# Kernel tuning notes

Hardware: AMD Instinct MI355X
Metric: run time of the kernel (lower is better)

Reference implementation:

```python
import jax, jax.numpy as jnp
import numpy as np

N = 16384        # num_nodes (64 graphs x 256 nodes, consecutive blocks)
G = 64           # num_graphs = len(nodes_per_graph)
GENES = 12132    # num_genes (hardcoded in source)
E = 262144       # edges, avg degree 16
PER = 256        # nodes per graph


def setup_inputs() -> dict:
    key = jax.random.key(0)
    ks = jax.random.split(key, 12)
    x = jax.random.normal(ks[0], (N, GENES), dtype=jnp.float32)
    edge_index = jax.random.randint(ks[1], (2, E), 0, N, dtype=jnp.int32)
    # node i belongs to graph i // PER  (consecutive-block partition as in the source loop)
    graph_ids = jnp.repeat(jnp.arange(G, dtype=jnp.int32), PER)
    node_scales = jax.random.uniform(ks[2], (GENES,), dtype=jnp.float32, minval=0.5, maxval=1.5)
    gcn_weight = jax.random.normal(ks[3], (GENES, G), dtype=jnp.float32) / np.float32(np.sqrt(GENES))
    gcn_bias = jax.random.normal(ks[4], (G,), dtype=jnp.float32) * 0.01
    w1 = jax.random.normal(ks[5], (G, N), dtype=jnp.float32) / np.float32(np.sqrt(N))   # to_graph_layer [out,in]
    b1 = jax.random.normal(ks[6], (G,), dtype=jnp.float32) * 0.01
    final_means = jax.random.normal(ks[7], (G,), dtype=jnp.float32)
    final_scales = jax.random.uniform(ks[8], (G,), dtype=jnp.float32, minval=0.5, maxval=1.5)
    w2 = jax.random.normal(ks[9], (1, G), dtype=jnp.float32) / np.float32(np.sqrt(G))   # to_final_layer
    b2 = jax.random.normal(ks[10], (1,), dtype=jnp.float32) * 0.01
    return {
        "x": x, "edge_index": edge_index, "graph_ids": graph_ids,
        "node_scales": node_scales, "gcn_weight": gcn_weight, "gcn_bias": gcn_bias,
        "w1": w1, "b1": b1, "final_means": final_means, "final_scales": final_scales,
        "w2": w2, "b2": b2,
    }


def reference(x, edge_index, graph_ids, node_scales, gcn_weight, gcn_bias,
              w1, b1, final_means, final_scales, w2, b2):
    n = x.shape[0]
    x = x / node_scales                              # [N, GENES]
    xw = x @ gcn_weight                              # [N, G]  GCNConv linear (normalize=False)
    src, dst = edge_index[0], edge_index[1]
    # message passing: sum x_j over in-edges; '+ xw' realizes the explicitly-added self loops
    agg = jax.ops.segment_sum(xw[src], dst, num_segments=n) + xw + gcn_bias  # [N, G]
    # per-graph gather: node i takes column graph_ids[i] (vectorized form of the source loop)
    selected = jnp.take_along_axis(agg, graph_ids[:, None], axis=1)[:, 0]    # [N]
    # NOTE: the (selected - graph_means)/graph_scales in the source is dead code
    # (immediately overwritten by `x = selected_outputs`), so it is omitted.
    h = w1 @ selected + b1                           # [G]
    h = (h - final_means) / final_scales
    out = w2 @ h + b2                                # [1]
    return jax.nn.sigmoid(out)
```

## Files before the change

### kernel.cpp

```cpp
#include <hip/hip_runtime.h>
#include <hip/hip_bf16.h>

typedef unsigned short u16;
typedef unsigned int   u32;
typedef __attribute__((ext_vector_type(8))) short bf16x8;
typedef __attribute__((ext_vector_type(4))) float f32x4;
typedef __attribute__((ext_vector_type(4))) u32   u32x4;

#define GENES  12132
#define KPAD   12160
#define NROW   16384
#define GCOL   64
#define KTAIL  12096
#define CHUNKS32 380
#define KSPLIT 5
#define CPW    76

__device__ __forceinline__ u32 pack_hi(float x, float y) {
  return __builtin_amdgcn_perm(__float_as_uint(y), __float_as_uint(x), 0x07060302u);
}
__device__ __forceinline__ u32 pack_lo(float x, float y) {
  float lx = x - __uint_as_float(__float_as_uint(x) & 0xFFFF0000u);
  float ly = y - __uint_as_float(__float_as_uint(y) & 0xFFFF0000u);
  return pack_hi(lx, ly);
}
__device__ __forceinline__ void cvt8(const float* __restrict__ p, bf16x8& h8, bf16x8& l8) {
  const f32x4 a = *(const f32x4*)p;
  const f32x4 b = *(const f32x4*)(p + 4);
  u32x4 hv = { pack_hi(a[0], a[1]), pack_hi(a[2], a[3]),
               pack_hi(b[0], b[1]), pack_hi(b[2], b[3]) };
  u32x4 lv = { pack_lo(a[0], a[1]), pack_lo(a[2], a[3]),
               pack_lo(b[0], b[1]), pack_lo(b[2], b[3]) };
  h8 = __builtin_bit_cast(bf16x8, hv);
  l8 = __builtin_bit_cast(bf16x8, lv);
}

__global__ __launch_bounds__(256) void prep_all(
    const float* __restrict__ gw, const float* __restrict__ ns,
    const float* __restrict__ x,
    u16* __restrict__ Wth, u16* __restrict__ Wtl,
    float* __restrict__ xpad, float* __restrict__ hbuf) {
  const int bid = blockIdx.x;
  const int t   = threadIdx.x;
  if (bid < KPAD / 64) {
    __shared__ u16 th[64 * 72];
    __shared__ u16 tl[64 * 72];
    const int k0 = bid * 64;
#pragma unroll
    for (int i = 0; i < 16; ++i) {
      int idx = i * 256 + t;
      int k = idx >> 6, c = idx & 63;
      int gk = k0 + k;
      float wv = 0.f;
      if (gk < GENES) wv = gw[(size_t)gk * GCOL + c] / ns[gk];
      u32 u = __float_as_uint(wv);
      float lf = wv - __uint_as_float(u & 0xFFFF0000u);
      th[c * 72 + k] = (u16)(u >> 16);
      tl[c * 72 + k] = (u16)(__float_as_uint(lf) >> 16);
    }
    __syncthreads();
    const int c  = t >> 2;
    const int kk = (t & 3) * 16;
    uint4 a0 = *(const uint4*)(th + c * 72 + kk);
    uint4 a1 = *(const uint4*)(th + c * 72 + kk + 8);
    uint4 b0 = *(const uint4*)(tl + c * 72 + kk);
    uint4 b1 = *(const uint4*)(tl + c * 72 + kk + 8);
    *(uint4*)(Wth + (size_t)c * KPAD + k0 + kk)     = a0;
    *(uint4*)(Wth + (size_t)c * KPAD + k0 + kk + 8) = a1;
    *(uint4*)(Wtl + (size_t)c * KPAD + k0 + kk)     = b0;
    *(uint4*)(Wtl + (size_t)c * KPAD + k0 + kk + 8) = b1;
  } else {
    int i = (bid - KPAD / 64) * 256 + t;
    int row = i >> 6, col = i & 63;
    float v = 0.f;
    if (col < GENES - KTAIL) v = x[(size_t)row * GENES + KTAIL + col];
    xpad[i] = v;
    if (bid == KPAD / 64 && t < 64) hbuf[t] = 0.f;
  }
}

__global__ __launch_bounds__(64) void gemm_kernel(
    const float* __restrict__ x, const float* __restrict__ xpad,
    const u16* __restrict__ Wth, const u16* __restrict__ Wtl,
    float* __restrict__ xwp) {
  const int wid = blockIdx.x;
  const int sp  = wid >> 8;
  const int rg  = wid & 255;
  const int l   = threadIdx.x;
  const int lr  = l & 15;
  const int kq  = l >> 4;

  const int r0 = rg * 64;

  f32x4 acc[4][4];
#pragma unroll
  for (int s = 0; s < 4; ++s)
#pragma unroll
    for (int c = 0; c < 4; ++c) acc[s][c] = (f32x4){0.f, 0.f, 0.f, 0.f};

  const u16* bh_base = Wth + (size_t)lr * KPAD + kq * 8;
  const u16* bl_base = Wtl + (size_t)lr * KPAD + kq * 8;
  const int gch0 = sp * CPW;

#pragma unroll 2
  for (int ci = 0; ci < CPW; ++ci) {
    const int gch = gch0 + ci;
    const int k0  = gch * 32;
    bf16x8 bh[4], bl[4];
#pragma unroll
    for (int cg = 0; cg < 4; ++cg) {
      bh[cg] = *(const bf16x8*)(bh_base + (size_t)cg * (16 * KPAD) + k0);
      bl[cg] = *(const bf16x8*)(bl_base + (size_t)cg * (16 * KPAD) + k0);
    }
    bf16x8 ah[4], al[4];
    if (gch < KTAIL / 32) {
#pragma unroll
      for (int s = 0; s < 4; ++s)
        cvt8(x + (size_t)(r0 + s * 16 + lr) * GENES + k0 + kq * 8, ah[s], al[s]);
    } else {
#pragma unroll
      for (int s = 0; s < 4; ++s)
        cvt8(xpad + (size_t)(r0 + s * 16 + lr) * 64 + (k0 - KTAIL) + kq * 8, ah[s], al[s]);
    }
#pragma unroll
    for (int s = 0; s < 4; ++s)
#pragma unroll
      for (int cg = 0; cg < 4; ++cg) {
        acc[s][cg] = __builtin_amdgcn_mfma_f32_16x16x32_bf16(ah[s], bh[cg], acc[s][cg], 0, 0, 0);
        acc[s][cg] = __builtin_amdgcn_mfma_f32_16x16x32_bf16(al[s], bh[cg], acc[s][cg], 0, 0, 0);
        acc[s][cg] = __builtin_amdgcn_mfma_f32_16x16x32_bf16(ah[s], bl[cg], acc[s][cg], 0, 0, 0);
      }
  }

  float* outp = xwp + (size_t)sp * NROW * GCOL;
#pragma unroll
  for (int s = 0; s < 4; ++s) {
    const int rbase = r0 + s * 16 + kq * 4;
#pragma unroll
    for (int cg = 0; cg < 4; ++cg) {
      const int col = cg * 16 + lr;
#pragma unroll
      for (int j = 0; j < 4; ++j)
        outp[(size_t)(rbase + j) * GCOL + col] = acc[s][cg][j];
    }
  }
}

__global__ __launch_bounds__(256) void reduce_sel(
    const f32x4* __restrict__ xwp, f32x4* __restrict__ xw4,
    const float* __restrict__ gb, float* __restrict__ sel) {
  int i = blockIdx.x * 256 + threadIdx.x;
  f32x4 v = xwp[i];
#pragma unroll
  for (int p = 1; p < KSPLIT; ++p) {
    f32x4 u = xwp[(size_t)p * (NROW * GCOL / 4) + i];
    v[0] += u[0]; v[1] += u[1]; v[2] += u[2]; v[3] += u[3];
  }
  xw4[i] = v;
  int row = i >> 4;
  int g = row >> 8;
  if ((i & 15) == (g >> 2)) sel[row] = v[g & 3] + gb[g];
}

__global__ __launch_bounds__(256) void edge_kernel(
    const int* __restrict__ ei, const float* __restrict__ xw,
    float* __restrict__ sel, int E) {
  int e = blockIdx.x * 256 + threadIdx.x;
  if (e < E) {
    int s = ei[e];
    int d = ei[E + e];
    int g = d >> 8;
    atomicAdd(&sel[d], xw[(size_t)s * GCOL + g]);
  }
}

__global__ __launch_bounds__(256) void hreduce_kernel(
    const float* __restrict__ w1, const float* __restrict__ sel,
    float* __restrict__ hbuf) {
  const int k = blockIdx.x >> 2;
  const int q = blockIdx.x & 3;
  const int t = threadIdx.x;
  const float4* wr = reinterpret_cast<const float4*>(w1 + (size_t)k * NROW);
  const float4* sv = reinterpret_cast<const float4*>(sel);
  float sum = 0.f;
#pragma unroll
  for (int i = 0; i < 4; ++i) {
    int idx = q * 1024 + i * 256 + t;
    float4 a = wr[idx];
    float4 b = sv[idx];
    sum += a.x * b.x + a.y * b.y + a.z * b.z + a.w * b.w;
  }
#pragma unroll
  for (int off = 32; off > 0; off >>= 1) sum += __shfl_down(sum, off, 64);
  __shared__ float wsum[4];
  if ((t & 63) == 0) wsum[t >> 6] = sum;
  __syncthreads();
  if (t == 0) atomicAdd(&hbuf[k], wsum[0] + wsum[1] + wsum[2] + wsum[3]);
}

__global__ void finalize_kernel(
    const float* __restrict__ hbuf, const float* __restrict__ b1,
    const float* __restrict__ fm, const float* __restrict__ fs,
    const float* __restrict__ w2, const float* __restrict__ b2,
    float* __restrict__ out) {
  int t = threadIdx.x;
  float h  = hbuf[t] + b1[t];
  float hn = (h - fm[t]) / fs[t];
  float v  = w2[t] * hn;
#pragma unroll
  for (int off = 32; off > 0; off >>= 1) v += __shfl_down(v, off, 64);
  if (t == 0) {
    float z = v + b2[0];
    out[0] = 1.f / (1.f + expf(-z));
  }
}

extern "C" void kernel_launch(void* const* d_in, const int* in_sizes, int n_in,
                              void* d_out, int out_size, void* d_ws, size_t ws_size,
                              hipStream_t stream) {
  const float* x    = (const float*)d_in[0];
  const int*   ei   = (const int*)d_in[1];
  const float* ns   = (const float*)d_in[3];
  const float* gw   = (const float*)d_in[4];
  const float* gb   = (const float*)d_in[5];
  const float* w1   = (const float*)d_in[6];
  const float* b1   = (const float*)d_in[7];
  const float* fm   = (const float*)d_in[8];
  const float* fs   = (const float*)d_in[9];
  const float* w2   = (const float*)d_in[10];
  const float* b2   = (const float*)d_in[11];
  float* out = (float*)d_out;

  const int E = in_sizes[1] / 2;

  float* ws   = (float*)d_ws;
  float* xw   = ws;
  float* sel  = xw + (size_t)NROW * GCOL;
  float* hbuf = sel + NROW;
  u16*   Wth  = (u16*)(hbuf + 64);
  u16*   Wtl  = Wth + (size_t)GCOL * KPAD;
  float* xpad = (float*)(Wtl + (size_t)GCOL * KPAD);
  float* xwp  = xpad + (size_t)NROW * 64;

  hipLaunchKernelGGL(prep_all, dim3(KPAD / 64 + NROW * 64 / 256), dim3(256), 0, stream,
                     gw, ns, x, Wth, Wtl, xpad, hbuf);
  hipLaunchKernelGGL(gemm_kernel, dim3(256 * KSPLIT), dim3(64), 0, stream,
                     x, xpad, Wth, Wtl, xwp);
  hipLaunchKernelGGL(reduce_sel, dim3(NROW * GCOL / 4 / 256), dim3(256), 0, stream,
                     (const f32x4*)xwp, (f32x4*)xw, gb, sel);
  hipLaunchKernelGGL(edge_kernel, dim3((E + 255) / 256), dim3(256), 0, stream,
                     ei, xw, sel, E);
  hipLaunchKernelGGL(hreduce_kernel, dim3(GCOL * 4), dim3(256), 0, stream,
                     w1, sel, hbuf);
  hipLaunchKernelGGL(finalize_kernel, dim3(1), dim3(64), 0, stream,
                     hbuf, b1, fm, fs, w2, b2, out);
}
```

Before: 345.7 us.

## Prefetch next A chunk into registers and double the K-split

The GEMM loop now loads the next 32-wide K chunk of x into registers before running the current chunk's MFMAs, so global-load latency overlaps with compute. The K dimension is also split into 10 slices instead of 5, giving twice as many workgroups for occupancy. In exchange there are more partial-sum buffers to reduce afterwards and higher register pressure from the prefetch registers. The first chunk's load always reads x directly, which is correct only if no split begins in the padded tail.

```diff
diff --git a/kernel.cpp b/kernel.cpp
--- a/kernel.cpp
+++ b/kernel.cpp
@@ -12,9 +12,8 @@
 #define NROW   16384
 #define GCOL   64
 #define KTAIL  12096
-#define CHUNKS32 380
-#define KSPLIT 5
-#define CPW    76
+#define KSPLIT 10
+#define CPW    38
 
 __device__ __forceinline__ u32 pack_hi(float x, float y) {
   return __builtin_amdgcn_perm(__float_as_uint(y), __float_as_uint(x), 0x07060302u);
@@ -24,9 +23,7 @@
   float ly = y - __uint_as_float(__float_as_uint(y) & 0xFFFF0000u);
   return pack_hi(lx, ly);
 }
-__device__ __forceinline__ void cvt8(const float* __restrict__ p, bf16x8& h8, bf16x8& l8) {
-  const f32x4 a = *(const f32x4*)p;
-  const f32x4 b = *(const f32x4*)(p + 4);
+__device__ __forceinline__ void cvt8v(f32x4 a, f32x4 b, bf16x8& h8, bf16x8& l8) {
   u32x4 hv = { pack_hi(a[0], a[1]), pack_hi(a[2], a[3]),
                pack_hi(b[0], b[1]), pack_hi(b[2], b[3]) };
   u32x4 lv = { pack_lo(a[0], a[1]), pack_lo(a[2], a[3]),
@@ -89,8 +86,7 @@
   const int l   = threadIdx.x;
   const int lr  = l & 15;
   const int kq  = l >> 4;
-
-  const int r0 = rg * 64;
+  const int r0  = rg * 64;
 
   f32x4 acc[4][4];
 #pragma unroll
@@ -98,13 +94,24 @@
 #pragma unroll
     for (int c = 0; c < 4; ++c) acc[s][c] = (f32x4){0.f, 0.f, 0.f, 0.f};
 
-  const u16* bh_base = Wth + (size_t)lr * KPAD + kq * 8;
-  const u16* bl_base = Wtl + (size_t)lr * KPAD + kq * 8;
-  const int gch0 = sp * CPW;
-
-#pragma unroll 2
+  const u16*   bh_base = Wth + (size_t)lr * KPAD + kq * 8;
+  const u16*   bl_base = Wtl + (size_t)lr * KPAD + kq * 8;
+  const float* xbase   = x    + (size_t)(r0 + lr) * GENES + kq * 8;
+  const float* pbase   = xpad + (size_t)(r0 + lr) * 64    + kq * 8;
+  const int    c0      = sp * CPW;
+
+  f32x4 an[8];
+  {
+    const float* p = xbase + c0 * 32;
+#pragma unroll
+    for (int s = 0; s < 4; ++s) {
+      an[2 * s]     = *(const f32x4*)(p + (size_t)s * 16 * GENES);
+      an[2 * s + 1] = *(const f32x4*)(p + (size_t)s * 16 * GENES + 4);
+    }
+  }
+
   for (int ci = 0; ci < CPW; ++ci) {
-    const int gch = gch0 + ci;
+    const int gch = c0 + ci;
     const int k0  = gch * 32;
     bf16x8 bh[4], bl[4];
 #pragma unroll
@@ -113,14 +120,25 @@
       bl[cg] = *(const bf16x8*)(bl_base + (size_t)cg * (16 * KPAD) + k0);
     }
     bf16x8 ah[4], al[4];
-    if (gch < KTAIL / 32) {
-#pragma unroll
-      for (int s = 0; s < 4; ++s)
-        cvt8(x + (size_t)(r0 + s * 16 + lr) * GENES + k0 + kq * 8, ah[s], al[s]);
-    } else {
-#pragma unroll
-      for (int s = 0; s < 4; ++s)
-        cvt8(xpad + (size_t)(r0 + s * 16 + lr) * 64 + (k0 - KTAIL) + kq * 8, ah[s], al[s]);
+#pragma unroll
+    for (int s = 0; s < 4; ++s) cvt8v(an[2 * s], an[2 * s + 1], ah[s], al[s]);
+    if (ci + 1 < CPW) {
+      const int ngch = gch + 1;
+      if (ngch < KTAIL / 32) {
+        const float* p = xbase + ngch * 32;
+#pragma unroll
+        for (int s = 0; s < 4; ++s) {
+          an[2 * s]     = *(const f32x4*)(p + (size_t)s * 16 * GENES);
+          an[2 * s + 1] = *(const f32x4*)(p + (size_t)s * 16 * GENES + 4);
+        }
+      } else {
+        const float* p = pbase + (ngch * 32 - KTAIL);
+#pragma unroll
+        for (int s = 0; s < 4; ++s) {
+          an[2 * s]     = *(const f32x4*)(p + (size_t)s * 16 * 64);
+          an[2 * s + 1] = *(const f32x4*)(p + (size_t)s * 16 * 64 + 4);
+        }
+      }
     }
 #pragma unroll
     for (int s = 0; s < 4; ++s)
```

Result: no change. 346.5 us (+0.2%).

## Pre-swizzle weight fragments, use 4-wave blocks with A prefetch and deeper K-split

Applied to the files above, without the earlier changes.

The bf16 hi/lo weight split is now stored in MFMA-fragment order, so each lane does one contiguous 16-byte load per fragment instead of strided row reads. The GEMM moves from 64-thread blocks covering 64 rows to 256-thread blocks in which each wave covers 32 rows. The next A chunk is loaded before the current chunk's MFMAs are issued, and the K-split doubles to 10, which gives more blocks and more loads in flight for the memory-bound read of x. In exchange the partial-sum buffer and the reduce_sel traffic double, and the weight fragments are reloaded for every 32-row strip rather than every 64-row one.

```diff
diff --git a/kernel.cpp b/kernel.cpp
--- a/kernel.cpp
+++ b/kernel.cpp
@@ -12,9 +12,8 @@
 #define NROW   16384
 #define GCOL   64
 #define KTAIL  12096
-#define CHUNKS32 380
-#define KSPLIT 5
-#define CPW    76
+#define KSPLIT 10
+#define CPW    38
 
 __device__ __forceinline__ u32 pack_hi(float x, float y) {
   return __builtin_amdgcn_perm(__float_as_uint(y), __float_as_uint(x), 0x07060302u);
@@ -24,9 +23,7 @@
   float ly = y - __uint_as_float(__float_as_uint(y) & 0xFFFF0000u);
   return pack_hi(lx, ly);
 }
-__device__ __forceinline__ void cvt8(const float* __restrict__ p, bf16x8& h8, bf16x8& l8) {
-  const f32x4 a = *(const f32x4*)p;
-  const f32x4 b = *(const f32x4*)(p + 4);
+__device__ __forceinline__ void cvt8v(f32x4 a, f32x4 b, bf16x8& h8, bf16x8& l8) {
   u32x4 hv = { pack_hi(a[0], a[1]), pack_hi(a[2], a[3]),
                pack_hi(b[0], b[1]), pack_hi(b[2], b[3]) };
   u32x4 lv = { pack_lo(a[0], a[1]), pack_lo(a[2], a[3]),
@@ -38,8 +35,7 @@
 __global__ __launch_bounds__(256) void prep_all(
     const float* __restrict__ gw, const float* __restrict__ ns,
     const float* __restrict__ x,
-    u16* __restrict__ Wth, u16* __restrict__ Wtl,
-    float* __restrict__ xpad, float* __restrict__ hbuf) {
+    u16* __restrict__ B2, float* __restrict__ xpad, float* __restrict__ hbuf) {
   const int bid = blockIdx.x;
   const int t   = threadIdx.x;
   if (bid < KPAD / 64) {
@@ -59,16 +55,19 @@
       tl[c * 72 + k] = (u16)(__float_as_uint(lf) >> 16);
     }
     __syncthreads();
-    const int c  = t >> 2;
-    const int kk = (t & 3) * 16;
-    uint4 a0 = *(const uint4*)(th + c * 72 + kk);
-    uint4 a1 = *(const uint4*)(th + c * 72 + kk + 8);
-    uint4 b0 = *(const uint4*)(tl + c * 72 + kk);
-    uint4 b1 = *(const uint4*)(tl + c * 72 + kk + 8);
-    *(uint4*)(Wth + (size_t)c * KPAD + k0 + kk)     = a0;
-    *(uint4*)(Wth + (size_t)c * KPAD + k0 + kk + 8) = a1;
-    *(uint4*)(Wtl + (size_t)c * KPAD + k0 + kk)     = b0;
-    *(uint4*)(Wtl + (size_t)c * KPAD + k0 + kk + 8) = b1;
+#pragma unroll
+    for (int i = 0; i < 4; ++i) {
+      int idx = i * 256 + t;
+      int ch2 = idx >> 9;
+      int cg  = (idx >> 7) & 3;
+      int pl  = (idx >> 6) & 1;
+      int l   = idx & 63;
+      int c   = cg * 16 + (l & 15);
+      int klo = ch2 * 32 + (l >> 4) * 8;
+      const u16* src = (pl ? tl : th) + c * 72 + klo;
+      u16* dst = B2 + ((size_t)((bid * 2 + ch2) * 8 + cg * 2 + pl) * 64 + l) * 8;
+      *(uint4*)dst = *(const uint4*)src;
+    }
   } else {
     int i = (bid - KPAD / 64) * 256 + t;
     int row = i >> 6, col = i & 63;
@@ -79,69 +78,78 @@
   }
 }
 
-__global__ __launch_bounds__(64) void gemm_kernel(
+__global__ __launch_bounds__(256, 4) void gemm_kernel(
     const float* __restrict__ x, const float* __restrict__ xpad,
-    const u16* __restrict__ Wth, const u16* __restrict__ Wtl,
-    float* __restrict__ xwp) {
-  const int wid = blockIdx.x;
-  const int sp  = wid >> 8;
-  const int rg  = wid & 255;
-  const int l   = threadIdx.x;
-  const int lr  = l & 15;
-  const int kq  = l >> 4;
-
-  const int r0 = rg * 64;
-
-  f32x4 acc[4][4];
-#pragma unroll
-  for (int s = 0; s < 4; ++s)
-#pragma unroll
-    for (int c = 0; c < 4; ++c) acc[s][c] = (f32x4){0.f, 0.f, 0.f, 0.f};
-
-  const u16* bh_base = Wth + (size_t)lr * KPAD + kq * 8;
-  const u16* bl_base = Wtl + (size_t)lr * KPAD + kq * 8;
-  const int gch0 = sp * CPW;
-
-#pragma unroll 2
+    const u16* __restrict__ B2, float* __restrict__ xwp) {
+  const int sp = blockIdx.x >> 7;
+  const int rg = blockIdx.x & 127;
+  const int w  = threadIdx.x >> 6;
+  const int l  = threadIdx.x & 63;
+  const int lr = l & 15;
+  const int kq = l >> 4;
+  const int r0 = rg * 128 + w * 32;
+
+  f32x4 acc[2][4];
+#pragma unroll
+  for (int m = 0; m < 2; ++m)
+#pragma unroll
+    for (int c = 0; c < 4; ++c) acc[m][c] = (f32x4){0.f, 0.f, 0.f, 0.f};
+
+  const float* a0 = x    + (size_t)(r0 + lr) * GENES + kq * 8;
+  const float* p0 = xpad + (size_t)(r0 + lr) * 64    + kq * 8;
+  const int c0 = sp * CPW;
+
+  f32x4 an0a, an0b, an1a, an1b;
+  auto LOADA = [&](int gch) {
+    if (gch < KTAIL / 32) {
+      const float* q0 = a0 + gch * 32;
+      const float* q1 = q0 + (size_t)16 * GENES;
+      an0a = *(const f32x4*)q0;  an0b = *(const f32x4*)(q0 + 4);
+      an1a = *(const f32x4*)q1;  an1b = *(const f32x4*)(q1 + 4);
+    } else {
+      const float* q0 = p0 + (gch * 32 - KTAIL);
+      const float* q1 = q0 + 16 * 64;
+      an0a = *(const f32x4*)q0;  an0b = *(const f32x4*)(q0 + 4);
+      an1a = *(const f32x4*)q1;  an1b = *(const f32x4*)(q1 + 4);
+    }
+  };
+
+  LOADA(c0);
+
   for (int ci = 0; ci < CPW; ++ci) {
-    const int gch = gch0 + ci;
-    const int k0  = gch * 32;
+    const int gch = c0 + ci;
+    const u16* bp = B2 + (size_t)gch * 4096 + l * 8;
     bf16x8 bh[4], bl[4];
 #pragma unroll
     for (int cg = 0; cg < 4; ++cg) {
-      bh[cg] = *(const bf16x8*)(bh_base + (size_t)cg * (16 * KPAD) + k0);
-      bl[cg] = *(const bf16x8*)(bl_base + (size_t)cg * (16 * KPAD) + k0);
-    }
-    bf16x8 ah[4], al[4];
-    if (gch < KTAIL / 32) {
-#pragma unroll
-      for (int s = 0; s < 4; ++s)
-        cvt8(x + (size_t)(r0 + s * 16 + lr) * GENES + k0 + kq * 8, ah[s], al[s]);
-    } else {
-#pragma unroll
-      for (int s = 0; s < 4; ++s)
-        cvt8(xpad + (size_t)(r0 + s * 16 + lr) * 64 + (k0 - KTAIL) + kq * 8, ah[s], al[s]);
-    }
-#pragma unroll
-    for (int s = 0; s < 4; ++s)
-#pragma unroll
-      for (int cg = 0; cg < 4; ++cg) {
-        acc[s][cg] = __builtin_amdgcn_mfma_f32_16x16x32_bf16(ah[s], bh[cg], acc[s][cg], 0, 0, 0);
-        acc[s][cg] = __builtin_amdgcn_mfma_f32_16x16x32_bf16(al[s], bh[cg], acc[s][cg], 0, 0, 0);
-        acc[s][cg] = __builtin_amdgcn_mfma_f32_16x16x32_bf16(ah[s], bl[cg], acc[s][cg], 0, 0, 0);
-      }
+      bh[cg] = *(const bf16x8*)(bp + (cg * 2 + 0) * 512);
+      bl[cg] = *(const bf16x8*)(bp + (cg * 2 + 1) * 512);
+    }
+    bf16x8 ah0, al0, ah1, al1;
+    cvt8v(an0a, an0b, ah0, al0);
+    cvt8v(an1a, an1b, ah1, al1);
+    if (ci + 1 < CPW) LOADA(gch + 1);
+#pragma unroll
+    for (int cg = 0; cg < 4; ++cg) {
+      acc[0][cg] = __builtin_amdgcn_mfma_f32_16x16x32_bf16(ah0, bh[cg], acc[0][cg], 0, 0, 0);
+      acc[0][cg] = __builtin_amdgcn_mfma_f32_16x16x32_bf16(al0, bh[cg], acc[0][cg], 0, 0, 0);
+      acc[0][cg] = __builtin_amdgcn_mfma_f32_16x16x32_bf16(ah0, bl[cg], acc[0][cg], 0, 0, 0);
+      acc[1][cg] = __builtin_amdgcn_mfma_f32_16x16x32_bf16(ah1, bh[cg], acc[1][cg], 0, 0, 0);
+      acc[1][cg] = __builtin_amdgcn_mfma_f32_16x16x32_bf16(al1, bh[cg], acc[1][cg], 0, 0, 0);
+      acc[1][cg] = __builtin_amdgcn_mfma_f32_16x16x32_bf16(ah1, bl[cg], acc[1][cg], 0, 0, 0);
+    }
   }
 
   float* outp = xwp + (size_t)sp * NROW * GCOL;
 #pragma unroll
-  for (int s = 0; s < 4; ++s) {
-    const int rbase = r0 + s * 16 + kq * 4;
+  for (int m = 0; m < 2; ++m) {
+    const int rbase = r0 + m * 16 + kq * 4;
 #pragma unroll
     for (int cg = 0; cg < 4; ++cg) {
       const int col = cg * 16 + lr;
 #pragma unroll
       for (int j = 0; j < 4; ++j)
-        outp[(size_t)(rbase + j) * GCOL + col] = acc[s][cg][j];
+        outp[(size_t)(rbase + j) * GCOL + col] = acc[m][cg][j];
     }
   }
 }
@@ -237,15 +245,14 @@
   float* xw   = ws;
   float* sel  = xw + (size_t)NROW * GCOL;
   float* hbuf = sel + NROW;
-  u16*   Wth  = (u16*)(hbuf + 64);
-  u16*   Wtl  = Wth + (size_t)GCOL * KPAD;
-  float* xpad = (float*)(Wtl + (size_t)GCOL * KPAD);
+  u16*   B2   = (u16*)(hbuf + 64);
+  float* xpad = (float*)(B2 + (size_t)380 * 4096);
   float* xwp  = xpad + (size_t)NROW * 64;
 
   hipLaunchKernelGGL(prep_all, dim3(KPAD / 64 + NROW * 64 / 256), dim3(256), 0, stream,
-                     gw, ns, x, Wth, Wtl, xpad, hbuf);
-  hipLaunchKernelGGL(gemm_kernel, dim3(256 * KSPLIT), dim3(64), 0, stream,
-                     x, xpad, Wth, Wtl, xwp);
+                     gw, ns, x, B2, xpad, hbuf);
+  hipLaunchKernelGGL(gemm_kernel, dim3(128 * KSPLIT), dim3(256), 0, stream,
+                     x, xpad, B2, xwp);
   hipLaunchKernelGGL(reduce_sel, dim3(NROW * GCOL / 4 / 256), dim3(256), 0, stream,
                      (const f32x4*)xwp, (f32x4*)xw, gb, sel);
   hipLaunchKernelGGL(edge_kernel, dim3((E + 255) / 256), dim3(256), 0, stream,
```

After: 299.7 us. 13.3% less time.
